# Performance work log

Hardware: AMD Instinct MI355X
Metric: run time of the kernel (lower is better)

The kernel has to match this reference:

```python
import jax, jax.numpy as jnp
import numpy as np

LN_EPS = 1e-5

def _layer_norm(y, g, b):
    mu = y.mean(-1, keepdims=True)
    var = y.var(-1, keepdims=True)
    return (y - mu) * jax.lax.rsqrt(var + LN_EPS) * g + b

def setup_inputs() -> dict:
    key = jax.random.key(0)
    ks = jax.random.split(key, 10)
    F, D, H = 32, 128, 128
    FD = F * D
    B = 8192
    def rn(k, shape, fan_in):
        return jax.random.normal(k, shape, dtype=jnp.float32) / np.sqrt(fan_in)
    return {
        "x":   jax.random.normal(ks[0], (B, F), dtype=jnp.float32),
        "Wp":  rn(ks[1], (F, D), 1), "bp": jnp.zeros((F, D), jnp.float32),
        "fW1": rn(ks[2], (F, D, H), D), "fb1": jnp.zeros((F, H), jnp.float32),
        "fW2": rn(ks[3], (F, H, D), H), "fb2": jnp.zeros((F, D), jnp.float32),
        "fWg": rn(ks[4], (F, D, 2 * D), D), "fbg": jnp.zeros((F, 2 * D), jnp.float32),
        "fg":  jnp.ones((F, D), jnp.float32), "fbe": jnp.zeros((F, D), jnp.float32),
        "sW1": rn(ks[5], (FD, H), FD), "sb1": jnp.zeros((H,), jnp.float32),
        "sW2": rn(ks[6], (H, FD), H), "sb2": jnp.zeros((FD,), jnp.float32),
        "sWg": rn(ks[7], (FD, 2 * FD), FD), "sbg": jnp.zeros((2 * FD,), jnp.float32),
        "sg":  jnp.ones((FD,), jnp.float32), "sbe": jnp.zeros((FD,), jnp.float32),
        "Wh":  rn(ks[8], (FD, F), FD), "bh": jnp.zeros((F,), jnp.float32),
    }

def reference(x, Wp, bp, fW1, fb1, fW2, fb2, fWg, fbg, fg, fbe,
              sW1, sb1, sW2, sb2, sWg, sbg, sg, sbe, Wh, bh):
    B, F = x.shape
    D = Wp.shape[1]
    # per-feature Linear(1, d_model), batched over all features: (B, F, D)
    emb = x[:, :, None] * Wp[None] + bp[None]
    # per-feature GRNs, batched via einsum over the feature axis
    h = jax.nn.elu(jnp.einsum('bfd,fdh->bfh', emb, fW1) + fb1)
    h = jnp.einsum('bfh,fhd->bfd', h, fW2) + fb2
    gates = jnp.einsum('bfd,fde->bfe', h, fWg) + fbg          # (B, F, 2D)
    a, s = jnp.split(gates, 2, axis=-1)
    stacked = _layer_norm(emb + a * jax.nn.sigmoid(s), fg, fbe)  # (B, F, D)
    # selection GRN over the flattened embeddings
    flat = stacked.reshape(B, F * D)
    hh = jax.nn.elu(flat @ sW1 + sb1)
    hh = hh @ sW2 + sb2
    sgate = flat_gate = hh @ sWg + sbg                          # (B, 2FD)
    sa, ss = jnp.split(sgate, 2, axis=-1)
    sel_in = _layer_norm(flat + sa * jax.nn.sigmoid(ss), sg, sbe)
    weights = jax.nn.softmax(sel_in @ Wh + bh, axis=-1)        # (B, F)
    selected = jnp.einsum('bfd,bf->bd', stacked, weights)      # (B, D)
    return selected, weights
```

## Files before the change

kernel.cpp:

```cpp
#include <hip/hip_runtime.h>
#include <hip/hip_bf16.h>
#include <math.h>

#define BB 8192
#define FF 32
#define DD 128
#define HH 128
#define FD 4096
#define E2 256
#define F2 8192
#define LN_EPS 1e-5f
#define L2E 1.44269504f

typedef __hip_bfloat16 bf16;
typedef __attribute__((ext_vector_type(8))) short bf16x8;
typedef __attribute__((ext_vector_type(4))) float f32x4;

__device__ __forceinline__ float s2f(short s) {
  union { float f; unsigned u; } x; x.u = ((unsigned)(unsigned short)s) << 16; return x.f;
}
__device__ __forceinline__ short f2s(float v) {
  bf16 h = __float2bfloat16(v); return *(short*)&h;
}
__device__ __forceinline__ float fast_sigmoid(float s) {
  return __builtin_amdgcn_rcpf(1.f + __builtin_amdgcn_exp2f(-L2E * s));
}
__device__ __forceinline__ float fast_elu(float v) {
  return v > 0.f ? v : __builtin_amdgcn_exp2f(L2E * v) - 1.f;
}


__global__ void prep_A1(const float* __restrict__ Wp, const float* __restrict__ bp,
                        const float* __restrict__ fW1, const float* __restrict__ fb1,
                        float* __restrict__ A1, float* __restrict__ C1) {
  int f = blockIdx.x, h = threadIdx.x;
  const float* w1 = fW1 + (size_t)f * DD * HH;
  float a = 0.f, c = 0.f;
  for (int d = 0; d < DD; ++d) {
    float w = w1[d * HH + h];
    a += Wp[f * DD + d] * w;
    c += bp[f * DD + d] * w;
  }
  A1[f * HH + h] = a;
  C1[f * HH + h] = c + fb1[f * HH + h];
}

__global__ void prep_M2(const float* __restrict__ fW2, const float* __restrict__ fWg,
                        float* __restrict__ M2) {
  int f = blockIdx.x, h = blockIdx.y, e = threadIdx.x;
  const float* w2 = fW2 + ((size_t)f * HH + h) * DD;
  const float* wg = fWg + (size_t)f * DD * E2;
  float acc = 0.f;
  for (int d = 0; d < DD; ++d) acc += w2[d] * wg[d * E2 + e];
  M2[((size_t)f * HH + h) * E2 + e] = acc;
}

__global__ void m2_castT(const float* __restrict__ M2, short* __restrict__ M2T) {
  __shared__ float T[64][65];
  int h0 = blockIdx.x * 64, e0 = blockIdx.y * 64, f = blockIdx.z;
  int t = threadIdx.x;
  for (int i = 0; i < 16; ++i) {
    int idx = t + 256 * i; int r = idx >> 6, c = idx & 63;
    T[r][c] = M2[((size_t)f * HH + h0 + r) * E2 + e0 + c];
  }
  __syncthreads();
  for (int i = 0; i < 16; ++i) {
    int idx = t + 256 * i; int e = idx >> 6, h = idx & 63;
    M2T[((size_t)f * E2 + e0 + e) * HH + h0 + h] = f2s(T[h][e]);
  }
}

__global__ void prep_c2(const float* __restrict__ fb2, const float* __restrict__ fWg,
                        const float* __restrict__ fbg, float* __restrict__ c2) {
  int f = blockIdx.x, e = threadIdx.x;
  const float* wg = fWg + (size_t)f * DD * E2;
  float acc = 0.f;
  for (int d = 0; d < DD; ++d) acc += fb2[f * DD + d] * wg[d * E2 + e];
  c2[f * E2 + e] = acc + fbg[f * E2 + e];
}

__global__ void cast_bf16(const float* __restrict__ in, short* __restrict__ out, int n) {
  int i = blockIdx.x * 256 + threadIdx.x;
  if (i < n) out[i] = f2s(in[i]);
}

__global__ void castT(const float* __restrict__ in, short* __restrict__ out, int R, int C) {
  __shared__ float T[64][65];
  int c0 = blockIdx.x * 64, r0 = blockIdx.y * 64;
  int t = threadIdx.x;
  for (int i = 0; i < 16; ++i) {
    int idx = t + 256 * i; int r = idx >> 6, c = idx & 63;
    T[r][c] = in[(size_t)(r0 + r) * C + c0 + c];
  }
  __syncthreads();
  for (int i = 0; i < 16; ++i) {
    int idx = t + 256 * i; int c = idx >> 6, r = idx & 63;
    out[(size_t)(c0 + c) * R + r0 + r] = f2s(T[r][c]);
  }
}

__global__ void init_misc(const float* __restrict__ sbg, const float* __restrict__ bh,
                          float* __restrict__ c3, float* __restrict__ u,
                          float* __restrict__ w0) {
  int j = blockIdx.x * 256 + threadIdx.x;
  c3[j] = sbg[j];
  if (j < 32) { u[j] = 0.f; w0[j] = bh[j]; }
}

__global__ void castT_c3(const float* __restrict__ in, short* __restrict__ out,
                         const float* __restrict__ sb2, float* __restrict__ c3) {
  __shared__ float T[64][65];
  int c0 = blockIdx.x * 64, r0 = blockIdx.y * 64;
  int t = threadIdx.x;
  for (int i = 0; i < 16; ++i) {
    int idx = t + 256 * i; int r = idx >> 6, c = idx & 63;
    T[r][c] = in[(size_t)(r0 + r) * F2 + c0 + c];
  }
  __syncthreads();
  for (int i = 0; i < 16; ++i) {
    int idx = t + 256 * i; int c = idx >> 6, r = idx & 63;
    out[(size_t)(c0 + c) * FD + r0 + r] = f2s(T[r][c]);
  }
  if (t < 64) {
    float s = 0.f;
    for (int r = 0; r < 64; ++r) s += sb2[r0 + r] * T[r][t];
    atomicAdd(&c3[c0 + t], s);
  }
}

__global__ void prep_whs(const float* __restrict__ Wh, const float* __restrict__ sg,
                         const float* __restrict__ sbe, short* __restrict__ WhS,
                         float* __restrict__ u, float* __restrict__ w0) {
  __shared__ float T[64][33];
  int k0 = blockIdx.x * 64;
  int t = threadIdx.x;
  {
    int k = t >> 5, c = t & 31;
    for (int i = 0; i < 8; ++i)
      T[k + 8 * i][c] = Wh[(size_t)(k0 + k + 8 * i) * FF + c];
  }
  __syncthreads();
  {
    int c = t >> 3, kk = (t & 7) * 8;
    short o[8];
    for (int i = 0; i < 8; ++i) o[i] = f2s(sg[k0 + kk + i] * T[kk + i][c]);
    *(bf16x8*)&WhS[(size_t)c * FD + k0 + kk] = *(bf16x8*)&o[0];
  }
  if (t < 32) {
    float su = 0.f, sw = 0.f;
    for (int k = 0; k < 64; ++k) { su += sg[k0 + k] * T[k][t]; sw += sbe[k0 + k] * T[k][t]; }
    atomicAdd(&u[t], su);
    atomicAdd(&w0[t], sw);
  }
}

__global__ __launch_bounds__(256) void gemm_bt_n128_splitk(
    const short* __restrict__ A, const short* __restrict__ BT,
    float* __restrict__ Cp, int M, int K) {
  __shared__ short As[128 * 72];
  __shared__ short Bs[128 * 72];
  int m0 = blockIdx.x * 128;
  int kchunk = K >> 2;
  int kbase = blockIdx.y * kchunk;
  int tid = threadIdx.x;
  int lane = tid & 63, w = tid >> 6;
  int wm = (w >> 1) * 64, wn = (w & 1) * 64;
  int lm = lane & 15, lq = lane >> 4;
  f32x4 acc[4][4] = {};
  for (int kc = 0; kc < kchunk; kc += 64) {
    for (int i = 0; i < 4; ++i) {
      int li = tid + 256 * i;
      int r = li >> 3, c8 = (li & 7) * 8;
      *(bf16x8*)&As[r * 72 + c8] = *(const bf16x8*)&A[(size_t)(m0 + r) * K + kbase + kc + c8];
      *(bf16x8*)&Bs[r * 72 + c8] = *(const bf16x8*)&BT[(size_t)r * K + kbase + kc + c8];
    }
    __syncthreads();
    for (int ks = 0; ks < 2; ++ks) {
      bf16x8 af[4], bfr[4];
      for (int i = 0; i < 4; ++i)
        af[i] = *(const bf16x8*)&As[(wm + i * 16 + lm) * 72 + ks * 32 + lq * 8];
      for (int j = 0; j < 4; ++j)
        bfr[j] = *(const bf16x8*)&Bs[(wn + j * 16 + lm) * 72 + ks * 32 + lq * 8];
      for (int i = 0; i < 4; ++i)
        for (int j = 0; j < 4; ++j)
          acc[i][j] = __builtin_amdgcn_mfma_f32_16x16x32_bf16(af[i], bfr[j], acc[i][j], 0, 0, 0);
    }
    __syncthreads();
  }
  float* out = Cp + (size_t)blockIdx.y * M * 128;
  for (int i = 0; i < 4; ++i)
    for (int j = 0; j < 4; ++j)
      for (int v = 0; v < 4; ++v) {
        int r = wm + i * 16 + lq * 4 + v;
        int c = wn + j * 16 + lm;
        out[(size_t)(m0 + r) * 128 + c] = acc[i][j][v];
      }
}

__global__ void reduce_m3t(const float* __restrict__ Cp, short* __restrict__ M3T, int M) {
  size_t i = (size_t)blockIdx.x * 256 + threadIdx.x;
  float s = 0.f;
  for (int k = 0; k < 4; ++k) s += Cp[(size_t)k * M * 128 + i];
  M3T[i] = f2s(s);
}

__global__ void reduce_hh1(const float* __restrict__ Cp, const float* __restrict__ sb1,
                           short* __restrict__ hh1, int M) {
  size_t i = (size_t)blockIdx.x * 256 + threadIdx.x;
  float s = 0.f;
  for (int k = 0; k < 4; ++k) s += Cp[(size_t)k * M * 128 + i];
  s += sb1[i & 127];
  hh1[i] = f2s(fast_elu(s));
}

__global__ __launch_bounds__(256) void stageA_mfma(
    const float* __restrict__ x, const float* __restrict__ Wp,
    const float* __restrict__ bp, const float* __restrict__ A1,
    const float* __restrict__ C1, const short* __restrict__ M2T,
    const float* __restrict__ c2, const float* __restrict__ fg,
    const float* __restrict__ fbe, short* __restrict__ stacked) {
  __shared__ __align__(16) char SM[3 * 128 * 72 * 2];
  short* As = (short*)SM;
  short* Ba = (short*)(SM + 128 * 72 * 2);
  short* Bb = (short*)(SM + 2 * 128 * 72 * 2);
  short* Co = (short*)(SM + 128 * 72 * 2);
  __shared__ float xsh[128];
  __shared__ float red[2][128][2];
  int f = blockIdx.y;
  int m0 = blockIdx.x * 128;
  int tid = threadIdx.x;
  int lane = tid & 63, w = tid >> 6;
  int wm = (w >> 1) * 64, wn = (w & 1) * 64;
  int lm = lane & 15, lq = lane >> 4;
  if (tid < 128) xsh[tid] = x[(size_t)(m0 + tid) * FF + f];
  __syncthreads();
  f32x4 accA[4][4] = {}, accB[4][4] = {};
  for (int kc = 0; kc < HH; kc += 64) {
    {
      int r = tid >> 1;
      int hcb = (tid & 1) * 32;
      float xr = xsh[r];
      const float* a1p = A1 + f * HH + kc + hcb;
      const float* c1p = C1 + f * HH + kc + hcb;
      short* dst = &As[r * 72 + hcb];
      for (int s = 0; s < 32; ++s) {
        float v = fmaf(xr, a1p[s], c1p[s]);
        dst[s] = f2s(fast_elu(v));
      }
    }
    for (int i = 0; i < 4; ++i) {
      int li = tid + 256 * i;
      int rr = li >> 3, c8 = (li & 7) * 8;
      *(bf16x8*)&Ba[rr * 72 + c8] = *(const bf16x8*)&M2T[((size_t)f * E2 + rr) * HH + kc + c8];
      *(bf16x8*)&Bb[rr * 72 + c8] = *(const bf16x8*)&M2T[((size_t)f * E2 + 128 + rr) * HH + kc + c8];
    }
    __syncthreads();
    for (int ks = 0; ks < 2; ++ks) {
      bf16x8 af[4], ba[4], bb[4];
      for (int i = 0; i < 4; ++i)
        af[i] = *(const bf16x8*)&As[(wm + i * 16 + lm) * 72 + ks * 32 + lq * 8];
      for (int j = 0; j < 4; ++j) {
        ba[j] = *(const bf16x8*)&Ba[(wn + j * 16 + lm) * 72 + ks * 32 + lq * 8];
        bb[j] = *(const bf16x8*)&Bb[(wn + j * 16 + lm) * 72 + ks * 32 + lq * 8];
      }
      for (int i = 0; i < 4; ++i)
        for (int j = 0; j < 4; ++j) {
          accA[i][j] = __builtin_amdgcn_mfma_f32_16x16x32_bf16(af[i], ba[j], accA[i][j], 0, 0, 0);
          accB[i][j] = __builtin_amdgcn_mfma_f32_16x16x32_bf16(af[i], bb[j], accB[i][j], 0, 0, 0);
        }
    }
    __syncthreads();
  }
  float c2a[4], c2s[4], wpv[4], bpv[4];
  for (int j = 0; j < 4; ++j) {
    int c = wn + j * 16 + lm;
    c2a[j] = c2[f * E2 + c];
    c2s[j] = c2[f * E2 + 128 + c];
    wpv[j] = Wp[f * DD + c];
    bpv[j] = bp[f * DD + c];
  }
  for (int i = 0; i < 4; ++i)
    for (int v = 0; v < 4; ++v) {
      int r = wm + i * 16 + lq * 4 + v;
      float xr = xsh[r];
      float sum = 0.f, sq = 0.f;
      for (int j = 0; j < 4; ++j) {
        float a = accA[i][j][v] + c2a[j];
        float s = accB[i][j][v] + c2s[j];
        float emb = fmaf(xr, wpv[j], bpv[j]);
        float y = fmaf(a, fast_sigmoid(s), emb);
        accA[i][j][v] = y;
        sum += y; sq += y * y;
      }
      for (int m = 1; m < 16; m <<= 1) {
        sum += __shfl_xor(sum, m, 64);
        sq += __shfl_xor(sq, m, 64);
      }
      if (lm == 0) { red[w & 1][r][0] = sum; red[w & 1][r][1] = sq; }
    }
  __syncthreads();
  float fgv[4], fbev[4];
  for (int j = 0; j < 4; ++j) {
    int c = wn + j * 16 + lm;
    fgv[j] = fg[f * DD + c];
    fbev[j] = fbe[f * DD + c];
  }
  for (int i = 0; i < 4; ++i)
    for (int v = 0; v < 4; ++v) {
      int r = wm + i * 16 + lq * 4 + v;
      float tot = red[0][r][0] + red[1][r][0];
      float totq = red[0][r][1] + red[1][r][1];
      float mu = tot * (1.f / DD);
      float var = totq * (1.f / DD) - mu * mu;
      float rstd = rsqrtf(var + LN_EPS);
      for (int j = 0; j < 4; ++j) {
        int c = wn + j * 16 + lm;
        Co[r * 128 + c] = f2s((accA[i][j][v] - mu) * rstd * fgv[j] + fbev[j]);
      }
    }
  __syncthreads();
  for (int i = 0; i < 8; ++i) {
    int lin = tid + 256 * i;
    int r = lin >> 4, c8 = (lin & 15) * 8;
    *(bf16x8*)&stacked[((size_t)(m0 + r) * FF + f) * DD + c8] = *(bf16x8*)&Co[r * 128 + c8];
  }
}

__global__ __launch_bounds__(256) void sgate_mfma(
    const short* __restrict__ hh1, const short* __restrict__ M3T,
    const float* __restrict__ c3, const short* __restrict__ stacked,
    short* __restrict__ tmp) {
  __shared__ short As[128 * 72];
  __shared__ short Ba[64 * 72];
  __shared__ short Bb[64 * 72];
  short* Co = As;
  int m0 = blockIdx.x * 128;
  int c0 = blockIdx.y * 64;
  int tid = threadIdx.x;
  int lane = tid & 63, w = tid >> 6;
  int wm = (w >> 1) * 64, wn = (w & 1) * 32;
  int lm = lane & 15, lq = lane >> 4;
  f32x4 accA[4][2] = {}, accB[4][2] = {};
  for (int kc = 0; kc < 128; kc += 64) {
    for (int i = 0; i < 4; ++i) {
      int li = tid + 256 * i;
      int r = li >> 3, c8 = (li & 7) * 8;
      *(bf16x8*)&As[r * 72 + c8] = *(const bf16x8*)&hh1[(size_t)(m0 + r) * 128 + kc + c8];
    }
    for (int i = 0; i < 2; ++i) {
      int li = tid + 256 * i;
      int r = li >> 3, c8 = (li & 7) * 8;
      *(bf16x8*)&Ba[r * 72 + c8] = *(const bf16x8*)&M3T[(size_t)(c0 + r) * 128 + kc + c8];
      *(bf16x8*)&Bb[r * 72 + c8] = *(const bf16x8*)&M3T[(size_t)(4096 + c0 + r) * 128 + kc + c8];
    }
    __syncthreads();
    for (int ks = 0; ks < 2; ++ks) {
      bf16x8 af[4], ba[2], bb[2];
      for (int i = 0; i < 4; ++i)
        af[i] = *(const bf16x8*)&As[(wm + i * 16 + lm) * 72 + ks * 32 + lq * 8];
      for (int j = 0; j < 2; ++j) {
        ba[j] = *(const bf16x8*)&Ba[(wn + j * 16 + lm) * 72 + ks * 32 + lq * 8];
        bb[j] = *(const bf16x8*)&Bb[(wn + j * 16 + lm) * 72 + ks * 32 + lq * 8];
      }
      for (int i = 0; i < 4; ++i)
        for (int j = 0; j < 2; ++j) {
          accA[i][j] = __builtin_amdgcn_mfma_f32_16x16x32_bf16(af[i], ba[j], accA[i][j], 0, 0, 0);
          accB[i][j] = __builtin_amdgcn_mfma_f32_16x16x32_bf16(af[i], bb[j], accB[i][j], 0, 0, 0);
        }
    }
    __syncthreads();
  }
  for (int i = 0; i < 4; ++i)
    for (int j = 0; j < 2; ++j)
      for (int v = 0; v < 4; ++v) {
        int rl = wm + i * 16 + lq * 4 + v;
        int cl = wn + j * 16 + lm;
        int c = c0 + cl;
        float sa = accA[i][j][v] + c3[c];
        float ss = accB[i][j][v] + c3[c + 4096];
        Co[rl * 64 + cl] = f2s(sa * fast_sigmoid(ss));
      }
  __syncthreads();
  for (int i = 0; i < 4; ++i) {
    int lin = tid + 256 * i;
    int r = lin >> 3, c8 = (lin & 7) * 8;
    size_t gi = (size_t)(m0 + r) * FD + c0 + c8;
    bf16x8 sv = *(const bf16x8*)&stacked[gi];
    bf16x8 av = *(bf16x8*)&Co[r * 64 + c8];
    short ov[8];
    for (int e = 0; e < 8; ++e) ov[e] = f2s(s2f(sv[e]) + s2f(av[e]));
    *(bf16x8*)&tmp[gi] = *(bf16x8*)&ov[0];
  }
}

__global__ __launch_bounds__(256) void ln_stats2(const short* __restrict__ tmp,
                                                 float* __restrict__ rowstats) {
  int b = blockIdx.x;
  int t = threadIdx.x;
  const short* row = tmp + (size_t)b * FD;
  bf16x8 v0 = *(const bf16x8*)&row[t * 16];
  bf16x8 v1 = *(const bf16x8*)&row[t * 16 + 8];
  float sum = 0.f, sq = 0.f;
  for (int i = 0; i < 8; ++i) {
    float a = s2f(v0[i]), bv = s2f(v1[i]);
    sum += a + bv; sq += a * a + bv * bv;
  }
  for (int off = 32; off; off >>= 1) { sum += __shfl_down(sum, off); sq += __shfl_down(sq, off); }
  __shared__ float rs[4], rq[4];
  int wid = t >> 6;
  if ((t & 63) == 0) { rs[wid] = sum; rq[wid] = sq; }
  __syncthreads();
  if (t == 0) {
    float tot = rs[0] + rs[1] + rs[2] + rs[3];
    float totq = rq[0] + rq[1] + rq[2] + rq[3];
    float mu = tot * (1.f / FD);
    float var = totq * (1.f / FD) - mu * mu;
    rowstats[2 * b] = mu;
    rowstats[2 * b + 1] = rsqrtf(var + LN_EPS);
  }
}

__global__ __launch_bounds__(256) void gemm_logits_splitk(
    const short* __restrict__ tmp, const short* __restrict__ WhS,
    float* __restrict__ partial) {
  __shared__ short As[128 * 72];
  __shared__ short Bs[32 * 72];
  int m0 = blockIdx.x * 128;
  int kbase = blockIdx.y * (FD / 4);
  int tid = threadIdx.x;
  int lane = tid & 63, w = tid >> 6;
  int wm = w * 32;
  int lm = lane & 15, lq = lane >> 4;
  f32x4 acc[2][2] = {};
  for (int kc = 0; kc < FD / 4; kc += 64) {
    for (int i = 0; i < 4; ++i) {
      int li = tid + 256 * i;
      int r = li >> 3, c8 = (li & 7) * 8;
      *(bf16x8*)&As[r * 72 + c8] = *(const bf16x8*)&tmp[(size_t)(m0 + r) * FD + kbase + kc + c8];
    }
    {
      int r = tid >> 3, c8 = (tid & 7) * 8;
      *(bf16x8*)&Bs[r * 72 + c8] = *(const bf16x8*)&WhS[(size_t)r * FD + kbase + kc + c8];
    }
    __syncthreads();
    for (int ks = 0; ks < 2; ++ks) {
      bf16x8 af[2], bfr[2];
      for (int i = 0; i < 2; ++i)
        af[i] = *(const bf16x8*)&As[(wm + i * 16 + lm) * 72 + ks * 32 + lq * 8];
      for (int j = 0; j < 2; ++j)
        bfr[j] = *(const bf16x8*)&Bs[(j * 16 + lm) * 72 + ks * 32 + lq * 8];
      for (int i = 0; i < 2; ++i)
        for (int j = 0; j < 2; ++j)
          acc[i][j] = __builtin_amdgcn_mfma_f32_16x16x32_bf16(af[i], bfr[j], acc[i][j], 0, 0, 0);
    }
    __syncthreads();
  }
  for (int i = 0; i < 2; ++i)
    for (int j = 0; j < 2; ++j)
      for (int v = 0; v < 4; ++v) {
        int r = m0 + wm + i * 16 + lq * 4 + v;
        int c = j * 16 + lm;
        partial[(size_t)blockIdx.y * BB * FF + (size_t)r * FF + c] = acc[i][j][v];
      }
}

__global__ __launch_bounds__(128) void select_fused(
    const float* __restrict__ partial, const float* __restrict__ rowstats,
    const float* __restrict__ u, const float* __restrict__ w0,
    const short* __restrict__ stacked, float* __restrict__ outsel,
    float* __restrict__ outw) {
  __shared__ float wf[FF];
  __shared__ short L[FD];
  int b = blockIdx.x;
  int t = threadIdx.x;
  for (int i = 0; i < 4; ++i) {
    int idx = t + 128 * i;
    *(bf16x8*)&L[idx * 8] = *(const bf16x8*)&stacked[(size_t)b * FD + idx * 8];
  }
  if (t < 32) {
    float s = 0.f;
    for (int p = 0; p < 4; ++p) s += partial[(size_t)p * BB * FF + (size_t)b * FF + t];
    float mu = rowstats[2 * b], rstd = rowstats[2 * b + 1];
    float l = rstd * s - mu * rstd * u[t] + w0[t];
    float m = l;
    for (int off = 16; off; off >>= 1) m = fmaxf(m, __shfl_xor(m, off, 32));
    float e = __builtin_amdgcn_exp2f(L2E * (l - m));
    float ss = e;
    for (int off = 16; off; off >>= 1) ss += __shfl_xor(ss, off, 32);
    float wv = e / ss;
    wf[t] = wv;
    outw[(size_t)b * FF + t] = wv;
  }
  __syncthreads();
  float acc = 0.f;
  for (int ff = 0; ff < FF; ++ff) acc += s2f(L[ff * 128 + t]) * wf[ff];
  outsel[(size_t)b * DD + t] = acc;
}

extern "C" void kernel_launch(void* const* d_in, const int* in_sizes, int n_in,
                              void* d_out, int out_size, void* d_ws, size_t ws_size,
                              hipStream_t stream) {
  const float* x   = (const float*)d_in[0];
  const float* Wp  = (const float*)d_in[1];
  const float* bp  = (const float*)d_in[2];
  const float* fW1 = (const float*)d_in[3];
  const float* fb1 = (const float*)d_in[4];
  const float* fW2 = (const float*)d_in[5];
  const float* fb2 = (const float*)d_in[6];
  const float* fWg = (const float*)d_in[7];
  const float* fbg = (const float*)d_in[8];
  const float* fg  = (const float*)d_in[9];
  const float* fbe = (const float*)d_in[10];
  const float* sW1 = (const float*)d_in[11];
  const float* sb1 = (const float*)d_in[12];
  const float* sW2 = (const float*)d_in[13];
  const float* sb2 = (const float*)d_in[14];
  const float* sWg = (const float*)d_in[15];
  const float* sbg = (const float*)d_in[16];
  const float* sg  = (const float*)d_in[17];
  const float* sbe = (const float*)d_in[18];
  const float* Wh  = (const float*)d_in[19];
  const float* bh  = (const float*)d_in[20];

  float* w = (float*)d_ws;
  size_t off = 0;
  float* A1   = w + off; off += (size_t)FF * HH;
  float* C1   = w + off; off += (size_t)FF * HH;
  float* c2   = w + off; off += (size_t)FF * E2;
  float* c3   = w + off; off += (size_t)F2;
  float* rowstats = w + off; off += (size_t)2 * BB;
  float* u    = w + off; off += 32;
  float* w0   = w + off; off += 32;
  float* M2   = w + off; off += (size_t)FF * HH * E2;
  float* partial = w + off; off += (size_t)4 * BB * 128;
  short* hh1  = (short*)(w + off); off += (size_t)BB * 128 / 2;
  short* M3T  = (short*)(w + off); off += (size_t)F2 * 128 / 2;
  short* sW2b = (short*)(w + off); off += (size_t)128 * FD / 2;
  short* sW1T = (short*)(w + off); off += (size_t)128 * FD / 2;
  short* M2T  = (short*)(w + off); off += (size_t)FF * E2 * HH / 2;
  short* WhS  = (short*)(w + off); off += (size_t)FF * FD / 2;
  short* stacked = (short*)(w + off); off += (size_t)BB * FD / 2;
  short* tmp  = (short*)(w + off); off += (size_t)BB * FD / 2;
  short* sWgT = (short*)(w + off); off += (size_t)F2 * FD / 2;

  float* outsel = (float*)d_out;
  float* outw   = outsel + (size_t)BB * DD;

  cast_bf16<<<(128 * FD + 255) / 256, 256, 0, stream>>>(sW2, sW2b, 128 * FD);
  castT<<<dim3(DD / 64, FD / 64), 256, 0, stream>>>(sW1, sW1T, FD, DD);
  init_misc<<<F2 / 256, 256, 0, stream>>>(sbg, bh, c3, u, w0);
  castT_c3<<<dim3(F2 / 64, FD / 64), 256, 0, stream>>>(sWg, sWgT, sb2, c3);
  prep_whs<<<FD / 64, 256, 0, stream>>>(Wh, sg, sbe, WhS, u, w0);
  gemm_bt_n128_splitk<<<dim3(F2 / 128, 4), 256, 0, stream>>>(sWgT, sW2b, partial, F2, FD);
  reduce_m3t<<<(F2 * 128) / 256, 256, 0, stream>>>(partial, M3T, F2);
  prep_A1<<<FF, 128, 0, stream>>>(Wp, bp, fW1, fb1, A1, C1);
  prep_M2<<<dim3(FF, HH), E2, 0, stream>>>(fW2, fWg, M2);
  m2_castT<<<dim3(HH / 64, E2 / 64, FF), 256, 0, stream>>>(M2, M2T);
  prep_c2<<<FF, E2, 0, stream>>>(fb2, fWg, fbg, c2);
  stageA_mfma<<<dim3(BB / 128, FF), 256, 0, stream>>>(x, Wp, bp, A1, C1, M2T, c2, fg, fbe,
                                                      stacked);
  gemm_bt_n128_splitk<<<dim3(BB / 128, 4), 256, 0, stream>>>(stacked, sW1T, partial, BB, FD);
  reduce_hh1<<<(BB * 128) / 256, 256, 0, stream>>>(partial, sb1, hh1, BB);
  sgate_mfma<<<dim3(BB / 128, FD / 64), 256, 0, stream>>>(hh1, M3T, c3, stacked, tmp);
  ln_stats2<<<BB, 256, 0, stream>>>(tmp, rowstats);
  gemm_logits_splitk<<<dim3(BB / 128, 4), 256, 0, stream>>>(tmp, WhS, partial);
  select_fused<<<BB, 128, 0, stream>>>(partial, rowstats, u, w0, stacked, outsel, outw);
}
```

Measured before the change: 569.7 us.

## Swizzle stageA LDS tiles, vectorize ELU tile fill, batch LN shuffles

Replaces the padded 72-stride LDS tiles in stageA_mfma with 128-byte rows and an XOR swizzle. This removes bank conflicts without padding, and the LayerNorm reduction buffer now reuses the shared memory region, shrinking the LDS footprint. The ELU-activated A tile is now built with vectorized A1/C1 loads and 16-byte LDS stores instead of scalar short stores. The per-row shuffle reductions are batched across all rows to expose more instruction-level parallelism. A launch-bounds occupancy hint of 3 blocks per CU is added, which may cap registers and cause spills given the large accumulator arrays.

```diff
diff --git a/kernel.cpp b/kernel.cpp
--- a/kernel.cpp
+++ b/kernel.cpp
@@ -27,6 +27,10 @@
 }
 __device__ __forceinline__ float fast_elu(float v) {
   return v > 0.f ? v : __builtin_amdgcn_exp2f(L2E * v) - 1.f;
+}
+
+__device__ __forceinline__ int swz128x64(int row, int hb) {
+  return row * 128 + (hb ^ ((row & 7) << 4));
 }
 
 
@@ -213,19 +217,19 @@
   hh1[i] = f2s(fast_elu(s));
 }
 
-__global__ __launch_bounds__(256) void stageA_mfma(
+__global__ __launch_bounds__(256, 3) void stageA_mfma(
     const float* __restrict__ x, const float* __restrict__ Wp,
     const float* __restrict__ bp, const float* __restrict__ A1,
     const float* __restrict__ C1, const short* __restrict__ M2T,
     const float* __restrict__ c2, const float* __restrict__ fg,
     const float* __restrict__ fbe, short* __restrict__ stacked) {
-  __shared__ __align__(16) char SM[3 * 128 * 72 * 2];
-  short* As = (short*)SM;
-  short* Ba = (short*)(SM + 128 * 72 * 2);
-  short* Bb = (short*)(SM + 2 * 128 * 72 * 2);
-  short* Co = (short*)(SM + 128 * 72 * 2);
+  __shared__ __align__(16) char SM[3 * 128 * 64 * 2];
+  char* As = SM;
+  char* Ba = SM + 128 * 64 * 2;
+  char* Bb = SM + 2 * 128 * 64 * 2;
+  short* Co = (short*)(SM + 128 * 64 * 2);
+  float* red = (float*)SM;
   __shared__ float xsh[128];
-  __shared__ float red[2][128][2];
   int f = blockIdx.y;
   int m0 = blockIdx.x * 128;
   int tid = threadIdx.x;
@@ -235,33 +239,41 @@
   if (tid < 128) xsh[tid] = x[(size_t)(m0 + tid) * FF + f];
   __syncthreads();
   f32x4 accA[4][4] = {}, accB[4][4] = {};
+  int c8 = (tid & 7) * 8, rb = tid >> 3;
   for (int kc = 0; kc < HH; kc += 64) {
     {
-      int r = tid >> 1;
-      int hcb = (tid & 1) * 32;
-      float xr = xsh[r];
-      const float* a1p = A1 + f * HH + kc + hcb;
-      const float* c1p = C1 + f * HH + kc + hcb;
-      short* dst = &As[r * 72 + hcb];
-      for (int s = 0; s < 32; ++s) {
-        float v = fmaf(xr, a1p[s], c1p[s]);
-        dst[s] = f2s(fast_elu(v));
+      f32x4 a1lo = *(const f32x4*)&A1[f * HH + kc + c8];
+      f32x4 a1hi = *(const f32x4*)&A1[f * HH + kc + c8 + 4];
+      f32x4 c1lo = *(const f32x4*)&C1[f * HH + kc + c8];
+      f32x4 c1hi = *(const f32x4*)&C1[f * HH + kc + c8 + 4];
+      for (int rr = 0; rr < 4; ++rr) {
+        int row = rb + rr * 32;
+        float xr = xsh[row];
+        short o[8];
+        for (int e = 0; e < 4; ++e) {
+          o[e]     = f2s(fast_elu(fmaf(xr, a1lo[e], c1lo[e])));
+          o[e + 4] = f2s(fast_elu(fmaf(xr, a1hi[e], c1hi[e])));
+        }
+        *(bf16x8*)(As + swz128x64(row, c8 * 2)) = *(bf16x8*)&o[0];
       }
     }
     for (int i = 0; i < 4; ++i) {
       int li = tid + 256 * i;
-      int rr = li >> 3, c8 = (li & 7) * 8;
-      *(bf16x8*)&Ba[rr * 72 + c8] = *(const bf16x8*)&M2T[((size_t)f * E2 + rr) * HH + kc + c8];
-      *(bf16x8*)&Bb[rr * 72 + c8] = *(const bf16x8*)&M2T[((size_t)f * E2 + 128 + rr) * HH + kc + c8];
+      int r = li >> 3, cc = (li & 7) * 8;
+      bf16x8 va = *(const bf16x8*)&M2T[((size_t)f * E2 + r) * HH + kc + cc];
+      bf16x8 vb = *(const bf16x8*)&M2T[((size_t)f * E2 + 128 + r) * HH + kc + cc];
+      *(bf16x8*)(Ba + swz128x64(r, cc * 2)) = va;
+      *(bf16x8*)(Bb + swz128x64(r, cc * 2)) = vb;
     }
     __syncthreads();
     for (int ks = 0; ks < 2; ++ks) {
       bf16x8 af[4], ba[4], bb[4];
+      int hb = ks * 64 + lq * 16;
       for (int i = 0; i < 4; ++i)
-        af[i] = *(const bf16x8*)&As[(wm + i * 16 + lm) * 72 + ks * 32 + lq * 8];
+        af[i] = *(const bf16x8*)(As + swz128x64(wm + i * 16 + lm, hb));
       for (int j = 0; j < 4; ++j) {
-        ba[j] = *(const bf16x8*)&Ba[(wn + j * 16 + lm) * 72 + ks * 32 + lq * 8];
-        bb[j] = *(const bf16x8*)&Bb[(wn + j * 16 + lm) * 72 + ks * 32 + lq * 8];
+        ba[j] = *(const bf16x8*)(Ba + swz128x64(wn + j * 16 + lm, hb));
+        bb[j] = *(const bf16x8*)(Bb + swz128x64(wn + j * 16 + lm, hb));
       }
       for (int i = 0; i < 4; ++i)
         for (int j = 0; j < 4; ++j) {
@@ -279,6 +291,7 @@
     wpv[j] = Wp[f * DD + c];
     bpv[j] = bp[f * DD + c];
   }
+  float rs[4][4], rq[4][4];
   for (int i = 0; i < 4; ++i)
     for (int v = 0; v < 4; ++v) {
       int r = wm + i * 16 + lq * 4 + v;
@@ -292,12 +305,21 @@
         accA[i][j][v] = y;
         sum += y; sq += y * y;
       }
-      for (int m = 1; m < 16; m <<= 1) {
-        sum += __shfl_xor(sum, m, 64);
-        sq += __shfl_xor(sq, m, 64);
-      }
-      if (lm == 0) { red[w & 1][r][0] = sum; red[w & 1][r][1] = sq; }
-    }
+      rs[i][v] = sum; rq[i][v] = sq;
+    }
+  for (int m = 1; m < 16; m <<= 1)
+    for (int i = 0; i < 4; ++i)
+      for (int v = 0; v < 4; ++v) {
+        rs[i][v] += __shfl_xor(rs[i][v], m, 64);
+        rq[i][v] += __shfl_xor(rq[i][v], m, 64);
+      }
+  if (lm == 0)
+    for (int i = 0; i < 4; ++i)
+      for (int v = 0; v < 4; ++v) {
+        int r = wm + i * 16 + lq * 4 + v;
+        red[(w & 1) * 256 + r * 2]     = rs[i][v];
+        red[(w & 1) * 256 + r * 2 + 1] = rq[i][v];
+      }
   __syncthreads();
   float fgv[4], fbev[4];
   for (int j = 0; j < 4; ++j) {
@@ -308,8 +330,8 @@
   for (int i = 0; i < 4; ++i)
     for (int v = 0; v < 4; ++v) {
       int r = wm + i * 16 + lq * 4 + v;
-      float tot = red[0][r][0] + red[1][r][0];
-      float totq = red[0][r][1] + red[1][r][1];
+      float tot  = red[r * 2]     + red[256 + r * 2];
+      float totq = red[r * 2 + 1] + red[256 + r * 2 + 1];
       float mu = tot * (1.f / DD);
       float var = totq * (1.f / DD) - mu * mu;
       float rstd = rsqrtf(var + LN_EPS);
@@ -321,8 +343,8 @@
   __syncthreads();
   for (int i = 0; i < 8; ++i) {
     int lin = tid + 256 * i;
-    int r = lin >> 4, c8 = (lin & 15) * 8;
-    *(bf16x8*)&stacked[((size_t)(m0 + r) * FF + f) * DD + c8] = *(bf16x8*)&Co[r * 128 + c8];
+    int r = lin >> 4, cc8 = (lin & 15) * 8;
+    *(bf16x8*)&stacked[((size_t)(m0 + r) * FF + f) * DD + cc8] = *(bf16x8*)&Co[r * 128 + cc8];
   }
 }
 
```

Result: slower. 589.5 us (+3.5%).
